# Kernel tuning notes

Hardware: AMD Instinct MI355X
Metric: run time of the kernel (lower is better)

The kernel has to match this reference:

```python
import jax, jax.numpy as jnp
import numpy as np

N = 4096   # nodes
G = 64     # graphs
MH = 128   # hidden multiplicity (0e and 1o)
MU = 64    # up multiplicity (0e and 1o)
NSP = 10   # num_species
EPS = 1e-5


def _forward(nfh, nfu, onehot, W_h0, W_h1, W_u0, W_u1, Wt_00, Wt_11, Wt_01, Wt_10,
             W_p0, b_p0, W_p1, Wsc0, Wsc1, ln_w0, ln_b0, ln_w1, W_s0, b_s0, W_s1, batch):
    n = nfh.shape[0]
    # unpack irreps layout: [0e scalars | 1o vectors flattened]
    h0 = nfh[:, :MH]                       # [N, MH]
    h1 = nfh[:, MH:].reshape(n, MH, 3)     # [N, MH, 3]
    u0 = nfu[:, :MU]
    u1 = nfu[:, MU:].reshape(n, MU, 3)
    inv_h = 1.0 / np.sqrt(MH)
    inv_u = 1.0 / np.sqrt(MU)
    # irrep-wise (block-diagonal) o3.Linear, e3nn fan-in normalization
    hp0 = (h0 @ W_h0) * inv_h
    hp1 = jnp.einsum('nui,uv->nvi', h1, W_h1) * inv_h
    up0 = (u0 @ W_u0) * inv_u
    up1 = jnp.einsum('nui,uv->nvi', u1, W_u1) * inv_u
    # SeparateWeightTensorProduct: fully-connected 'uvw' CG tensor product
    # paths to 0e (scalars + gates, 2*MH outputs): 0e x 0e and 1o x 1o (dot / sqrt3)
    inv_tp = 1.0 / np.sqrt(2.0 * MH * MU)   # component/path normalization (2 paths, fan MH*MU)
    xy00 = jnp.einsum('nu,nv->nuv', hp0, up0).reshape(n, MH * MU)
    xy11 = jnp.einsum('nui,nvi->nuv', hp1, up1).reshape(n, MH * MU)
    z0 = (xy00 @ Wt_00.reshape(MH * MU, 2 * MH)
          + (xy11 @ Wt_11.reshape(MH * MU, 2 * MH)) / np.sqrt(3.0)) * inv_tp  # [N, 2*MH]
    # paths to 1o: 0e x 1o and 1o x 0e (staged to control intermediate size)
    ta = jnp.einsum('nu,uvw->nvw', hp0, Wt_01)       # [N, MU, MH]
    z1a = jnp.einsum('nvw,nvi->nwi', ta, up1)
    tb = jnp.einsum('nv,uvw->nuw', up0, Wt_10)       # [N, MH, MH]
    z1b = jnp.einsum('nuw,nui->nwi', tb, hp1)
    z1 = (z1a + z1b) * inv_tp                        # [N, MH, 3]
    # Gate nonlinearity: silu on scalars, sigmoid gates multiply 1o features
    s = jax.nn.silu(z0[:, :MH])
    g = jax.nn.sigmoid(z0[:, MH:])
    v = z1 * g[:, :, None]
    # lin_post (biases on scalars only)
    p0 = (s @ W_p0) * inv_h + b_p0
    p1 = jnp.einsum('nui,uv->nvi', v, W_p1) * inv_h
    # self-connection: FullyConnectedTensorProduct(hidden, NSPx0e, out)
    inv_sc = 1.0 / np.sqrt(MH * NSP)
    sxy0 = jnp.einsum('nu,nv->nuv', h0, onehot).reshape(n, MH * NSP)
    y0 = p0 + (sxy0 @ Wsc0.reshape(MH * NSP, MH)) * inv_sc
    sxy1 = jnp.einsum('nui,nv->nuvi', h1, onehot).reshape(n, MH * NSP, 3)
    y1 = p1 + jnp.einsum('nki,kw->nwi', sxy1, Wsc1.reshape(MH * NSP, MH)) * inv_sc
    # e3LayerNorm: per-graph stats; mean-subtract scalars only, RMS-normalize per irrep
    ones = jnp.ones((n,), y0.dtype)
    cnt = jnp.maximum(jax.ops.segment_sum(ones, batch, num_segments=G), 1.0)[:, None]
    mean0 = (jax.ops.segment_sum(y0, batch, num_segments=G) / cnt).mean(axis=1)  # [G]
    f0 = y0 - mean0[batch][:, None]
    var0 = (jax.ops.segment_sum(f0 * f0, batch, num_segments=G) / cnt).mean(axis=1)
    f0 = f0 / (jnp.sqrt(var0)[batch][:, None] + EPS) * ln_w0 + ln_b0
    var1 = (jax.ops.segment_sum((y1 * y1).reshape(n, -1), batch, num_segments=G) / cnt).mean(axis=1)
    f1 = y1 / (jnp.sqrt(var1)[batch][:, None, None] + EPS) * ln_w1[None, :, None]
    # residual skip connection (o3.Linear with scalar bias)
    out0 = f0 + (h0 @ W_s0) * inv_h + b_s0
    out1 = f1 + jnp.einsum('nui,uv->nvi', h1, W_s1) * inv_h
    return jnp.concatenate([out0, out1.reshape(n, 3 * MH)], axis=1)  # [N, 512]


def setup_inputs() -> dict:
    key = jax.random.key(0)
    ks = jax.random.split(key, 20)
    f = lambda i, shape: jax.random.normal(ks[i], shape, dtype=jnp.float32)
    species = jax.random.randint(ks[0], (N,), 0, NSP)
    return {
        'node_feats_hidden': f(1, (N, 4 * MH)),
        'node_feats_up': f(2, (N, 4 * MU)),
        'node_one_hot': jax.nn.one_hot(species, NSP, dtype=jnp.float32),
        'batch': jnp.sort(jax.random.randint(ks[3], (N,), 0, G)),
        'W_h0': f(4, (MH, MH)), 'W_h1': f(5, (MH, MH)),
        'W_u0': f(6, (MU, MU)), 'W_u1': f(7, (MU, MU)),
        'Wt_00': f(8, (MH, MU, 2 * MH)), 'Wt_11': f(9, (MH, MU, 2 * MH)),
        'Wt_01': f(10, (MH, MU, MH)), 'Wt_10': f(11, (MH, MU, MH)),
        'W_p0': f(12, (MH, MH)), 'b_p0': jnp.zeros((MH,), jnp.float32), 'W_p1': f(13, (MH, MH)),
        'Wsc0': f(14, (MH, NSP, MH)), 'Wsc1': f(15, (MH, NSP, MH)),
        'ln_w0': jnp.ones((MH,), jnp.float32), 'ln_b0': jnp.zeros((MH,), jnp.float32),
        'ln_w1': jnp.ones((MH,), jnp.float32),
        'W_s0': f(16, (MH, MH)), 'b_s0': jnp.zeros((MH,), jnp.float32), 'W_s1': f(17, (MH, MH)),
    }


def reference(node_feats_hidden, node_feats_up, node_one_hot, batch, W_h0, W_h1, W_u0, W_u1,
              Wt_00, Wt_11, Wt_01, Wt_10, W_p0, b_p0, W_p1, Wsc0, Wsc1, ln_w0, ln_b0, ln_w1,
              W_s0, b_s0, W_s1):
    return _forward(node_feats_hidden, node_feats_up, node_one_hot, W_h0, W_h1, W_u0, W_u1,
                    Wt_00, Wt_11, Wt_01, Wt_10, W_p0, b_p0, W_p1, Wsc0, Wsc1,
                    ln_w0, ln_b0, ln_w1, W_s0, b_s0, W_s1, batch)
```

## Files before the change

kernel.cpp:

```cpp
#include <hip/hip_runtime.h>
#include <cstdint>
#include <cstddef>


typedef _Float16 half8 __attribute__((ext_vector_type(8)));
typedef _Float16 half4v __attribute__((ext_vector_type(4)));
typedef float f32x4 __attribute__((ext_vector_type(4)));

static constexpr float INV_H  = 0.08838834764831845f;
static constexpr float INV_U  = 0.125f;
static constexpr float INV_TP = 0.0078125f;
static constexpr float INV_SC = 0.02795084971874737f;
static constexpr float RSQRT3 = 0.5773502691896258f;
static constexpr float LN_EPS = 1e-5f;

static constexpr size_t OFF_BZ0 = 0;
static constexpr size_t OFF_BZ1 = OFF_BZ0 + 8388608;
static constexpr size_t OFF_WH0 = OFF_BZ1 + 4194304;
static constexpr size_t OFF_WH1 = OFF_WH0 + 32768;
static constexpr size_t OFF_WU0 = OFF_WH1 + 32768;
static constexpr size_t OFF_WU1 = OFF_WU0 + 8192;
static constexpr size_t OFF_WP0 = OFF_WU1 + 8192;
static constexpr size_t OFF_WP1 = OFF_WP0 + 32768;
static constexpr size_t OFF_WS0 = OFF_WP1 + 32768;
static constexpr size_t OFF_WS1 = OFF_WS0 + 32768;
static constexpr size_t OFF_H0F = OFF_WS1 + 32768;
static constexpr size_t OFF_H1F = OFF_H0F + 1048576;
static constexpr size_t OFF_U0F = OFF_H1F + 3145728;
static constexpr size_t OFF_U1F = OFF_U0F + 524288;
static constexpr size_t OFF_HP0 = OFF_U1F + 1572864;
static constexpr size_t OFF_HP1 = OFF_HP0 + 1048576;
static constexpr size_t OFF_UP0 = OFF_HP1 + 3145728;
static constexpr size_t OFF_UP1 = OFF_UP0 + 524288;
static constexpr size_t OFF_SF  = OFF_UP1 + 1572864;
static constexpr size_t OFF_VF  = OFF_SF + 1048576;
static constexpr size_t OFF_PZ0 = OFF_VF + 3145728;
static constexpr size_t OFF_PZ1 = OFF_PZ0 + 16777216;
static constexpr size_t OFF_Y0  = OFF_PZ1 + 12582912;
static constexpr size_t OFF_Y1  = OFF_Y0 + 2097152;
static constexpr size_t OFF_O0  = OFF_Y1 + 6291456;
static constexpr size_t OFF_O1  = OFF_O0 + 2097152;
static constexpr size_t OFF_SP  = OFF_O1 + 6291456;
static constexpr size_t OFF_ST  = OFF_SP + 16384;
static constexpr size_t WS_NEED = OFF_ST + 2048;

__global__ __launch_bounds__(256) void kconv(
    const float* __restrict__ nfh, const float* __restrict__ nfu,
    const float* __restrict__ onehot,
    const float* __restrict__ Wt00, const float* __restrict__ Wt11,
    const float* __restrict__ Wt01, const float* __restrict__ Wt10,
    const float* __restrict__ Wh0, const float* __restrict__ Wh1,
    const float* __restrict__ Wu0, const float* __restrict__ Wu1,
    const float* __restrict__ Wp0, const float* __restrict__ Wp1,
    const float* __restrict__ Ws0, const float* __restrict__ Ws1,
    char* __restrict__ ws)
{
  const int bid = blockIdx.x, t = threadIdx.x;
  if (bid < 768) {
    _Float16* dst;
    int u, nt = 0;
    const bool isz0 = bid < 512;
    if (isz0) { nt = bid >> 8; u = bid & 255; dst = (_Float16*)(ws + OFF_BZ0) + ((size_t)nt*256 + (size_t)u)*8192; }
    else      { u = bid - 512;               dst = (_Float16*)(ws + OFF_BZ1) + (size_t)u*8192; }
    for (int it = 0; it < 4; ++it) {
      int chunk = it*256 + t;
      int lane = chunk & 63, ch = chunk >> 6;
      int f = ch >> 1, c = ch & 1;
      int w = f*16 + (lane & 15);
      int v0 = c*32 + (lane >> 4)*8;
      half8 o;
      #pragma unroll
      for (int j = 0; j < 8; ++j) {
        float val;
        if (isz0) {
          if (u < 128) val = Wt00[(size_t)((u*64 + v0 + j)*256) + nt*128 + w];
          else         val = Wt11[(size_t)(((u-128)*64 + v0 + j)*256) + nt*128 + w] * RSQRT3;
        } else {
          if (u < 128) val = Wt01[(size_t)((u*64 + v0 + j)*128) + w];
          else         val = Wt10[(size_t)(((u-128)*64 + v0 + j)*128) + w];
        }
        o[j] = (_Float16)val;
      }
      *(half8*)(dst + (size_t)chunk*8) = o;
    }
  } else if (bid < 776) {
    int mat = bid - 768;
    const float* src; size_t doff; int K, N;
    switch (mat) {
      case 0: src = Wh0; doff = OFF_WH0; K = 128; N = 128; break;
      case 1: src = Wh1; doff = OFF_WH1; K = 128; N = 128; break;
      case 2: src = Wu0; doff = OFF_WU0; K = 64;  N = 64;  break;
      case 3: src = Wu1; doff = OFF_WU1; K = 64;  N = 64;  break;
      case 4: src = Wp0; doff = OFF_WP0; K = 128; N = 128; break;
      case 5: src = Wp1; doff = OFF_WP1; K = 128; N = 128; break;
      case 6: src = Ws0; doff = OFF_WS0; K = 128; N = 128; break;
      default: src = Ws1; doff = OFF_WS1; K = 128; N = 128; break;
    }
    _Float16* d = (_Float16*)(ws + doff);
    const int nfr = N >> 4;
    const int chunks = (K*N) >> 3;
    for (int qd = t; qd < chunks; qd += 256) {
      int lane = qd & 63, cf = qd >> 6;
      int f = cf % nfr, c = cf / nfr;
      int col = f*16 + (lane & 15);
      int k0 = c*32 + (lane >> 4)*8;
      half8 o;
      #pragma unroll
      for (int j = 0; j < 8; ++j) o[j] = (_Float16)src[(size_t)(k0 + j)*N + col];
      *(half8*)(d + (size_t)qd*8) = o;
    }
  } else if (bid < 1544) {
    const int stride = 768*256;
    const int base = (bid - 776)*256 + t;
    _Float16* h0f = (_Float16*)(ws + OFF_H0F);
    _Float16* h1f = (_Float16*)(ws + OFF_H1F);
    _Float16* u0f = (_Float16*)(ws + OFF_U0F);
    _Float16* u1f = (_Float16*)(ws + OFF_U1F);
    for (int id = base; id < 524288; id += stride)
      h0f[id] = (_Float16)nfh[(size_t)(id >> 7)*512 + (id & 127)];
    for (int id = base; id < 1572864; id += stride) {
      int i = id >> 19, r = id & 524287, n = r >> 7, u = r & 127;
      h1f[id] = (_Float16)nfh[(size_t)n*512 + 128 + u*3 + i];
    }
    for (int id = base; id < 262144; id += stride)
      u0f[id] = (_Float16)nfu[(size_t)(id >> 6)*256 + (id & 63)];
    for (int id = base; id < 786432; id += stride) {
      int i = id >> 18, r = id & 262143, n = r >> 6, v = r & 63;
      u1f[id] = (_Float16)nfu[(size_t)n*256 + 64 + v*3 + i];
    }
  } else {
    int node = (bid - 1544)*256 + t;
    const float* row = onehot + (size_t)node*10;
    int best = 0; float bv = row[0];
    #pragma unroll
    for (int s = 1; s < 10; ++s) { float v = row[s]; if (v > bv) { bv = v; best = s; } }
    ((int*)(ws + OFF_SP))[node] = best;
    if (bid == 1544) {
      float* stz = (float*)(ws + OFF_ST);
      stz[t] = 0.f; stz[t + 256] = 0.f;
    }
  }
}

template<int KK, int NO, int MODE>
__global__ __launch_bounds__(256) void kgemm_small(char* __restrict__ ws,
    const float* __restrict__ bp0, const float* __restrict__ bs0)
{
  constexpr int NT = NO / 16;
  const int bid = blockIdx.x, t = threadIdx.x;
  const int lane = t & 63, wid = t >> 6;
  const int quad = lane >> 4, l15 = lane & 15;
  const int job = bid >> 5, n0 = (bid & 31) << 7;

  const _Float16 *A, *W;
  _Float16* oh = nullptr; float* of = nullptr;
  const float* bias = nullptr;
  float scale;
  if constexpr (MODE == 0) {
    scale = INV_H;
    if (job == 0) { A = (const _Float16*)(ws + OFF_H0F); W = (const _Float16*)(ws + OFF_WH0); oh = (_Float16*)(ws + OFF_HP0); }
    else {
      A = (const _Float16*)(ws + OFF_H1F) + (size_t)(job-1)*524288;
      W = (const _Float16*)(ws + OFF_WH1);
      oh = (_Float16*)(ws + OFF_HP1) + (size_t)(job-1)*524288;
    }
  } else if constexpr (MODE == 1) {
    scale = INV_U;
    if (job == 0) { A = (const _Float16*)(ws + OFF_U0F); W = (const _Float16*)(ws + OFF_WU0); oh = (_Float16*)(ws + OFF_UP0); }
    else {
      A = (const _Float16*)(ws + OFF_U1F) + (size_t)(job-1)*262144;
      W = (const _Float16*)(ws + OFF_WU1);
      oh = (_Float16*)(ws + OFF_UP1) + (size_t)(job-1)*262144;
    }
  } else {
    scale = INV_H;
    switch (job) {
      case 0: A = (const _Float16*)(ws + OFF_SF);  W = (const _Float16*)(ws + OFF_WP0); of = (float*)(ws + OFF_Y0); bias = bp0; break;
      case 1: A = (const _Float16*)(ws + OFF_H0F); W = (const _Float16*)(ws + OFF_WS0); of = (float*)(ws + OFF_O0); bias = bs0; break;
      case 2: case 3: case 4:
        A = (const _Float16*)(ws + OFF_VF) + (size_t)(job-2)*524288;
        W = (const _Float16*)(ws + OFF_WP1);
        of = (float*)(ws + OFF_Y1) + (size_t)(job-2)*524288; break;
      default:
        A = (const _Float16*)(ws + OFF_H1F) + (size_t)(job-5)*524288;
        W = (const _Float16*)(ws + OFF_WS1);
        of = (float*)(ws + OFF_O1) + (size_t)(job-5)*524288; break;
    }
  }

  f32x4 acc[2][NT];
  const f32x4 zz = {0.f, 0.f, 0.f, 0.f};
  #pragma unroll
  for (int mf = 0; mf < 2; ++mf)
    #pragma unroll
    for (int nf = 0; nf < NT; ++nf) acc[mf][nf] = zz;

  #pragma unroll
  for (int kc = 0; kc < KK/32; ++kc) {
    half8 a[2];
    #pragma unroll
    for (int mf = 0; mf < 2; ++mf)
      a[mf] = *(const half8*)(A + (size_t)(n0 + wid*32 + mf*16 + l15)*KK + kc*32 + quad*8);
    #pragma unroll
    for (int nf = 0; nf < NT; ++nf) {
      half8 b = *(const half8*)(W + (size_t)(kc*NT + nf)*512 + lane*8);
      #pragma unroll
      for (int mf = 0; mf < 2; ++mf)
        acc[mf][nf] = __builtin_amdgcn_mfma_f32_16x16x32_f16(a[mf], b, acc[mf][nf], 0, 0, 0);
    }
  }

  #pragma unroll
  for (int mf = 0; mf < 2; ++mf)
    #pragma unroll
    for (int nf = 0; nf < NT; ++nf) {
      int col = nf*16 + l15;
      float bv = bias ? bias[col] : 0.f;
      #pragma unroll
      for (int r = 0; r < 4; ++r) {
        int row = n0 + wid*32 + mf*16 + quad*4 + r;
        float v = acc[mf][nf][r] * scale + bv;
        if constexpr (MODE < 2) oh[(size_t)row*NO + col] = (_Float16)v;
        else                    of[(size_t)row*NO + col] = v;
      }
    }
}

__global__ __launch_bounds__(256, 2) void kbig(char* __restrict__ ws)
{
  const int bid = blockIdx.x, t = threadIdx.x;
  const int lane = t & 63, wid = t >> 6;
  const int wy = wid >> 1, wx = wid & 1;
  const int quad = lane >> 4, l15 = lane & 15;

  const _Float16* hp0 = (const _Float16*)(ws + OFF_HP0);
  const _Float16* hp1 = (const _Float16*)(ws + OFF_HP1);
  const _Float16* up0 = (const _Float16*)(ws + OFF_UP0);
  const _Float16* up1 = (const _Float16*)(ws + OFF_UP1);

  const _Float16 *p, *q, *B0;
  float* out; int opitch; size_t obase; int node0;
  if (bid < 256) {
    int mt = bid >> 3, nt = (bid >> 2) & 1, kj = bid & 3;
    node0 = mt << 7;
    if (kj == 0) { p = hp0; q = up0; }
    else { p = hp1 + (size_t)(kj-1)*524288; q = up1 + (size_t)(kj-1)*262144; }
    B0 = (const _Float16*)(ws + OFF_BZ0) + (size_t)nt*2097152 + (kj ? (size_t)1048576 : (size_t)0);
    out = (float*)(ws + OFF_PZ0) + (size_t)kj*1048576;
    obase = (size_t)node0*256 + (size_t)nt*128;
    opitch = 256;
  } else {
    int b2 = bid - 256, mt = b2 >> 1, kj = b2 & 1, i = mt >> 5;
    node0 = (mt & 31) << 7;
    if (kj == 0) { p = hp0; q = up1 + (size_t)i*262144; }
    else         { p = hp1 + (size_t)i*524288; q = up0; }
    B0 = (const _Float16*)(ws + OFF_BZ1) + (kj ? (size_t)1048576 : (size_t)0);
    out = (float*)(ws + OFF_PZ1) + (size_t)kj*1572864;
    obase = (size_t)mt*16384;
    opitch = 128;
  }

  half8 qf[4][2];
  #pragma unroll
  for (int mf = 0; mf < 4; ++mf)
    #pragma unroll
    for (int c = 0; c < 2; ++c)
      qf[mf][c] = *(const half8*)(q + (size_t)(node0 + wy*64 + mf*16 + l15)*64 + c*32 + quad*8);

  f32x4 acc[4][4];
  const f32x4 zz = {0.f, 0.f, 0.f, 0.f};
  #pragma unroll
  for (int mf = 0; mf < 4; ++mf)
    #pragma unroll
    for (int nf = 0; nf < 4; ++nf) acc[mf][nf] = zz;

  const _Float16* prow = p + (size_t)(node0 + wy*64 + l15)*128;
  const _Float16* Bw = B0 + (size_t)wx*4096 + (size_t)lane*8;

  auto loadB = [&](half8 (&dst)[2][4], int uidx) {
    const _Float16* Bu = Bw + (size_t)uidx*8192;
    #pragma unroll
    for (int c = 0; c < 2; ++c)
      #pragma unroll
      for (int nf = 0; nf < 4; ++nf)
        dst[c][nf] = *(const half8*)(Bu + (size_t)((nf*2 + c)*512));
  };
  auto mstep = [&](const half8 (&bf)[2][4], const half4v (&pwl)[4], int uu) {
    #pragma unroll
    for (int mf = 0; mf < 4; ++mf) {
      const _Float16 ps = pwl[mf][uu];
      const half8 pv = {ps, ps, ps, ps, ps, ps, ps, ps};
      #pragma unroll
      for (int c = 0; c < 2; ++c) {
        half8 a = qf[mf][c] * pv;
        #pragma unroll
        for (int nf = 0; nf < 4; ++nf)
          acc[mf][nf] = __builtin_amdgcn_mfma_f32_16x16x32_f16(a, bf[c][nf], acc[mf][nf], 0, 0, 0);
      }
    }
  };

  half4v pw[4], pwN[4];
  #pragma unroll
  for (int mf = 0; mf < 4; ++mf)
    pw[mf] = *(const half4v*)(prow + (size_t)mf*2048);

  half8 bfA[2][4], bfB[2][4];
  loadB(bfA, 0);

  for (int u4 = 0; u4 < 32; ++u4) {
    const int b = u4*4;
    loadB(bfB, b + 1);
    mstep(bfA, pw, 0);
    loadB(bfA, b + 2);
    mstep(bfB, pw, 1);
    {
      const int np = (u4 < 31) ? (u4 + 1)*4 : u4*4;
      #pragma unroll
      for (int mf = 0; mf < 4; ++mf)
        pwN[mf] = *(const half4v*)(prow + (size_t)mf*2048 + np);
    }
    loadB(bfB, b + 3);
    mstep(bfA, pw, 2);
    loadB(bfA, (u4 < 31) ? (b + 4) : (b + 3));
    mstep(bfB, pw, 3);
    #pragma unroll
    for (int mf = 0; mf < 4; ++mf) pw[mf] = pwN[mf];
  }

  #pragma unroll
  for (int mf = 0; mf < 4; ++mf)
    #pragma unroll
    for (int nf = 0; nf < 4; ++nf) {
      int col = wx*64 + nf*16 + l15;
      #pragma unroll
      for (int r = 0; r < 4; ++r) {
        int row = wy*64 + mf*16 + quad*4 + r;
        out[obase + (size_t)row*opitch + col] = acc[mf][nf][r];
      }
    }
}

__global__ __launch_bounds__(256) void kreduce(char* __restrict__ ws)
{
  const int id = blockIdx.x*256 + threadIdx.x;
  const int n = id >> 7, w = id & 127;
  const float* pz0 = (const float*)(ws + OFF_PZ0);
  const float* pz1 = (const float*)(ws + OFF_PZ1);
  _Float16* sf = (_Float16*)(ws + OFF_SF);
  _Float16* vf = (_Float16*)(ws + OFF_VF);
  const size_t b = (size_t)n*256;
  float zs = (pz0[b + w] + pz0[1048576 + b + w] + pz0[2097152 + b + w] + pz0[3145728 + b + w]) * INV_TP;
  float zg = (pz0[b + 128 + w] + pz0[1048576 + b + 128 + w] + pz0[2097152 + b + 128 + w] + pz0[3145728 + b + 128 + w]) * INV_TP;
  float s = zs / (1.f + __expf(-zs));
  float g = 1.f / (1.f + __expf(-zg));
  sf[id] = (_Float16)s;
  #pragma unroll
  for (int i = 0; i < 3; ++i) {
    size_t r = ((size_t)i*4096 + (size_t)n)*128 + w;
    float z1v = (pz1[r] + pz1[1572864 + r]) * INV_TP;
    vf[(size_t)i*524288 + (size_t)n*128 + w] = (_Float16)(z1v * g);
  }
}

__global__ __launch_bounds__(256) void kscstats(char* __restrict__ ws,
    const float* __restrict__ nfh,
    const float* __restrict__ Wsc0, const float* __restrict__ Wsc1,
    const int* __restrict__ batch)
{
  const int t = threadIdx.x;
  const int node = blockIdx.x*2 + (t >> 7);
  const int w = t & 127;
  const int sp = ((const int*)(ws + OFF_SP))[node];
  const float* h = nfh + (size_t)node*512;
  float a0 = 0.f, a10 = 0.f, a11 = 0.f, a12 = 0.f;
  for (int u = 0; u < 128; ++u) {
    const size_t wi = (size_t)(u*10 + sp)*128 + w;
    float w0 = Wsc0[wi];
    float w1 = Wsc1[wi];
    a0 += h[u] * w0;
    a10 += h[128 + u*3 + 0] * w1;
    a11 += h[128 + u*3 + 1] * w1;
    a12 += h[128 + u*3 + 2] * w1;
  }
  float* y0 = (float*)(ws + OFF_Y0);
  float* y1 = (float*)(ws + OFF_Y1);
  const size_t i0 = (size_t)node*128 + w;
  float y0n  = y0[i0]           + INV_SC * a0;
  float y1n0 = y1[i0]           + INV_SC * a10;
  float y1n1 = y1[524288 + i0]  + INV_SC * a11;
  float y1n2 = y1[1048576 + i0] + INV_SC * a12;
  y0[i0] = y0n;
  y1[i0] = y1n0;
  y1[524288 + i0]  = y1n1;
  y1[1048576 + i0] = y1n2;

  float s0 = y0n, ss0 = y0n*y0n, ss1 = y1n0*y1n0 + y1n1*y1n1 + y1n2*y1n2;
  #pragma unroll
  for (int m = 1; m < 64; m <<= 1) {
    s0  += __shfl_xor(s0, m, 64);
    ss0 += __shfl_xor(ss0, m, 64);
    ss1 += __shfl_xor(ss1, m, 64);
  }
  __shared__ float red[4][3];
  if ((t & 63) == 0) {
    red[t >> 6][0] = s0; red[t >> 6][1] = ss0; red[t >> 6][2] = ss1;
  }
  __syncthreads();
  if ((t & 127) == 0) {
    const int wv = t >> 6;
    float* stp = (float*)(ws + OFF_ST);
    const int g = batch[node];
    atomicAdd(&stp[g],       red[wv][0] + red[wv+1][0]);
    atomicAdd(&stp[64 + g],  red[wv][1] + red[wv+1][1]);
    atomicAdd(&stp[128 + g], red[wv][2] + red[wv+1][2]);
    atomicAdd(&stp[192 + g], 1.f);
  }
}

__global__ __launch_bounds__(256) void kfinal(char* __restrict__ ws, const int* __restrict__ batch,
    const float* __restrict__ lnw0, const float* __restrict__ lnb0, const float* __restrict__ lnw1,
    float* __restrict__ outp)
{
  const int id = blockIdx.x*256 + threadIdx.x;
  const int n = id >> 9, c = id & 511;
  const float* st = (const float*)(ws + OFF_ST);
  const int g = batch[n];
  const float cnt = fmaxf(st[192 + g], 1.f);
  float val;
  if (c < 128) {
    const float* y0 = (const float*)(ws + OFF_Y0);
    const float* o0 = (const float*)(ws + OFF_O0);
    float m0   = st[g] / (cnt * 128.f);
    float var0 = st[64 + g] / (cnt * 128.f) - m0*m0;
    float inv0 = 1.f / (sqrtf(fmaxf(var0, 0.f)) + LN_EPS);
    val = (y0[(size_t)n*128 + c] - m0) * inv0 * lnw0[c] + lnb0[c] + o0[(size_t)n*128 + c];
  } else {
    int cc = c - 128, w = cc / 3, i = cc - w*3;
    const float* y1 = (const float*)(ws + OFF_Y1);
    const float* o1 = (const float*)(ws + OFF_O1);
    float inv1 = 1.f / (sqrtf(fmaxf(st[128 + g] / (cnt * 384.f), 0.f)) + LN_EPS);
    val = y1[(size_t)i*524288 + (size_t)n*128 + w] * inv1 * lnw1[w]
        + o1[(size_t)i*524288 + (size_t)n*128 + w];
  }
  outp[id] = val;
}

extern "C" void kernel_launch(void* const* d_in, const int* in_sizes, int n_in,
                              void* d_out, int out_size, void* d_ws, size_t ws_size,
                              hipStream_t stream)
{
  const float* nfh   = (const float*)d_in[0];
  const float* nfu   = (const float*)d_in[1];
  const float* oneh  = (const float*)d_in[2];
  const int*   batch = (const int*)d_in[3];
  const float* Wh0   = (const float*)d_in[4];
  const float* Wh1   = (const float*)d_in[5];
  const float* Wu0   = (const float*)d_in[6];
  const float* Wu1   = (const float*)d_in[7];
  const float* Wt00  = (const float*)d_in[8];
  const float* Wt11  = (const float*)d_in[9];
  const float* Wt01  = (const float*)d_in[10];
  const float* Wt10  = (const float*)d_in[11];
  const float* Wp0   = (const float*)d_in[12];
  const float* bp0   = (const float*)d_in[13];
  const float* Wp1   = (const float*)d_in[14];
  const float* Wsc0  = (const float*)d_in[15];
  const float* Wsc1  = (const float*)d_in[16];
  const float* lnw0  = (const float*)d_in[17];
  const float* lnb0  = (const float*)d_in[18];
  const float* lnw1  = (const float*)d_in[19];
  const float* Ws0   = (const float*)d_in[20];
  const float* bs0   = (const float*)d_in[21];
  const float* Ws1   = (const float*)d_in[22];
  char* ws = (char*)d_ws;

  if (ws_size < WS_NEED) {
    hipMemsetAsync(d_out, 0, (size_t)out_size * sizeof(float), stream);
    return;
  }

  kconv<<<1560, 256, 0, stream>>>(nfh, nfu, oneh, Wt00, Wt11, Wt01, Wt10,
                                  Wh0, Wh1, Wu0, Wu1, Wp0, Wp1, Ws0, Ws1, ws);
  kgemm_small<128,128,0><<<128, 256, 0, stream>>>(ws, nullptr, nullptr);
  kgemm_small<64, 64, 1><<<128, 256, 0, stream>>>(ws, nullptr, nullptr);
  kbig<<<448, 256, 0, stream>>>(ws);
  kreduce<<<2048, 256, 0, stream>>>(ws);
  kgemm_small<128,128,2><<<256, 256, 0, stream>>>(ws, bp0, bs0);
  kscstats<<<2048, 256, 0, stream>>>(ws, nfh, Wsc0, Wsc1, batch);
  kfinal<<<8192, 256, 0, stream>>>(ws, batch, lnw0, lnb0, lnw1, (float*)d_out);
}
```

Baseline: 353.8 us.

## Coalesce weight conversion via LDS, vectorize input casts, fp16 partials, merge small GEMMs

Weight repacking in kconv now stages each 64-row slab into LDS with float4 coalesced loads before the transposed fp16 pack, and the input casts use float4 loads and handle three vector components per thread. The two projection GEMMs are merged into one launch, and the big kernel writes its partial sums as fp16 instead of fp32, which halves the traffic into and out of kreduce. The hand-written double-buffered B prefetch in kbig is replaced by a simpler loop that leaves scheduling to the compiler. Storing partials in fp16 loses precision and risks overflow, and the simpler loop may hide less memory latency.

```diff
diff --git a/kernel.cpp b/kernel.cpp
--- a/kernel.cpp
+++ b/kernel.cpp
@@ -57,11 +57,34 @@
 {
   const int bid = blockIdx.x, t = threadIdx.x;
   if (bid < 768) {
+    __shared__ float lds[64 * 130];
     _Float16* dst;
     int u, nt = 0;
     const bool isz0 = bid < 512;
     if (isz0) { nt = bid >> 8; u = bid & 255; dst = (_Float16*)(ws + OFF_BZ0) + ((size_t)nt*256 + (size_t)u)*8192; }
     else      { u = bid - 512;               dst = (_Float16*)(ws + OFF_BZ1) + (size_t)u*8192; }
+
+    const float* src; int rowpitch, c0; float scale = 1.f;
+    if (isz0) {
+      rowpitch = 256; c0 = nt*128;
+      if (u < 128) { src = Wt00 + (size_t)(u*64)*256; }
+      else         { src = Wt11 + (size_t)((u-128)*64)*256; scale = RSQRT3; }
+    } else {
+      rowpitch = 128; c0 = 0;
+      if (u < 128) { src = Wt01 + (size_t)(u*64)*128; }
+      else         { src = Wt10 + (size_t)((u-128)*64)*128; }
+    }
+
+    #pragma unroll
+    for (int it = 0; it < 8; ++it) {
+      int gi = it*256 + t;
+      int row = gi >> 5, c4 = gi & 31;
+      const float4 v = *(const float4*)(src + (size_t)row*rowpitch + c0 + c4*4);
+      float* dl = lds + row*130 + c4*4;
+      dl[0] = v.x; dl[1] = v.y; dl[2] = v.z; dl[3] = v.w;
+    }
+    __syncthreads();
+
     for (int it = 0; it < 4; ++it) {
       int chunk = it*256 + t;
       int lane = chunk & 63, ch = chunk >> 6;
@@ -70,17 +93,8 @@
       int v0 = c*32 + (lane >> 4)*8;
       half8 o;
       #pragma unroll
-      for (int j = 0; j < 8; ++j) {
-        float val;
-        if (isz0) {
-          if (u < 128) val = Wt00[(size_t)((u*64 + v0 + j)*256) + nt*128 + w];
-          else         val = Wt11[(size_t)(((u-128)*64 + v0 + j)*256) + nt*128 + w] * RSQRT3;
-        } else {
-          if (u < 128) val = Wt01[(size_t)((u*64 + v0 + j)*128) + w];
-          else         val = Wt10[(size_t)(((u-128)*64 + v0 + j)*128) + w];
-        }
-        o[j] = (_Float16)val;
-      }
+      for (int j = 0; j < 8; ++j)
+        o[j] = (_Float16)(lds[(v0 + j)*130 + w] * scale);
       *(half8*)(dst + (size_t)chunk*8) = o;
     }
   } else if (bid < 776) {
@@ -116,17 +130,31 @@
     _Float16* h1f = (_Float16*)(ws + OFF_H1F);
     _Float16* u0f = (_Float16*)(ws + OFF_U0F);
     _Float16* u1f = (_Float16*)(ws + OFF_U1F);
-    for (int id = base; id < 524288; id += stride)
-      h0f[id] = (_Float16)nfh[(size_t)(id >> 7)*512 + (id & 127)];
-    for (int id = base; id < 1572864; id += stride) {
-      int i = id >> 19, r = id & 524287, n = r >> 7, u = r & 127;
-      h1f[id] = (_Float16)nfh[(size_t)n*512 + 128 + u*3 + i];
-    }
-    for (int id = base; id < 262144; id += stride)
-      u0f[id] = (_Float16)nfu[(size_t)(id >> 6)*256 + (id & 63)];
-    for (int id = base; id < 786432; id += stride) {
-      int i = id >> 18, r = id & 262143, n = r >> 6, v = r & 63;
-      u1f[id] = (_Float16)nfu[(size_t)n*256 + 64 + v*3 + i];
+    for (int vid = base; vid < 131072; vid += stride) {
+      int n = vid >> 5, c4 = (vid & 31)*4;
+      const float4 v = *(const float4*)(nfh + (size_t)n*512 + c4);
+      half4v o = { (_Float16)v.x, (_Float16)v.y, (_Float16)v.z, (_Float16)v.w };
+      *(half4v*)(h0f + (size_t)vid*4) = o;
+    }
+    for (int vid = base; vid < 65536; vid += stride) {
+      int n = vid >> 4, c4 = (vid & 15)*4;
+      const float4 v = *(const float4*)(nfu + (size_t)n*256 + c4);
+      half4v o = { (_Float16)v.x, (_Float16)v.y, (_Float16)v.z, (_Float16)v.w };
+      *(half4v*)(u0f + (size_t)vid*4) = o;
+    }
+    for (int id = base; id < 524288; id += stride) {
+      int n = id >> 7, u = id & 127;
+      const float* s = nfh + (size_t)n*512 + 128 + u*3;
+      h1f[id]            = (_Float16)s[0];
+      h1f[524288 + id]   = (_Float16)s[1];
+      h1f[1048576 + id]  = (_Float16)s[2];
+    }
+    for (int id = base; id < 262144; id += stride) {
+      int n = id >> 6, v = id & 63;
+      const float* s = nfu + (size_t)n*256 + 64 + v*3;
+      u1f[id]            = (_Float16)s[0];
+      u1f[262144 + id]   = (_Float16)s[1];
+      u1f[524288 + id]   = (_Float16)s[2];
     }
   } else {
     int node = (bid - 1544)*256 + t;
@@ -143,11 +171,11 @@
 }
 
 template<int KK, int NO, int MODE>
-__global__ __launch_bounds__(256) void kgemm_small(char* __restrict__ ws,
-    const float* __restrict__ bp0, const float* __restrict__ bs0)
+__device__ __forceinline__ void gemm_small_body(char* __restrict__ ws,
+    const float* __restrict__ bp0, const float* __restrict__ bs0,
+    int bid, int t)
 {
   constexpr int NT = NO / 16;
-  const int bid = blockIdx.x, t = threadIdx.x;
   const int lane = t & 63, wid = t >> 6;
   const int quad = lane >> 4, l15 = lane & 15;
   const int job = bid >> 5, n0 = (bid & 31) << 7;
@@ -226,6 +254,18 @@
     }
 }
 
+__global__ __launch_bounds__(256) void kprep(char* __restrict__ ws)
+{
+  if (blockIdx.x < 128) gemm_small_body<128,128,0>(ws, nullptr, nullptr, blockIdx.x, threadIdx.x);
+  else                  gemm_small_body<64, 64, 1>(ws, nullptr, nullptr, blockIdx.x - 128, threadIdx.x);
+}
+
+__global__ __launch_bounds__(256) void ktail(char* __restrict__ ws,
+    const float* __restrict__ bp0, const float* __restrict__ bs0)
+{
+  gemm_small_body<128,128,2>(ws, bp0, bs0, blockIdx.x, threadIdx.x);
+}
+
 __global__ __launch_bounds__(256, 2) void kbig(char* __restrict__ ws)
 {
   const int bid = blockIdx.x, t = threadIdx.x;
@@ -239,14 +279,14 @@
   const _Float16* up1 = (const _Float16*)(ws + OFF_UP1);
 
   const _Float16 *p, *q, *B0;
-  float* out; int opitch; size_t obase; int node0;
+  _Float16* out; int opitch; size_t obase; int node0;
   if (bid < 256) {
     int mt = bid >> 3, nt = (bid >> 2) & 1, kj = bid & 3;
     node0 = mt << 7;
     if (kj == 0) { p = hp0; q = up0; }
     else { p = hp1 + (size_t)(kj-1)*524288; q = up1 + (size_t)(kj-1)*262144; }
     B0 = (const _Float16*)(ws + OFF_BZ0) + (size_t)nt*2097152 + (kj ? (size_t)1048576 : (size_t)0);
-    out = (float*)(ws + OFF_PZ0) + (size_t)kj*1048576;
+    out = (_Float16*)(ws + OFF_PZ0) + (size_t)kj*1048576;
     obase = (size_t)node0*256 + (size_t)nt*128;
     opitch = 256;
   } else {
@@ -255,7 +295,7 @@
     if (kj == 0) { p = hp0; q = up1 + (size_t)i*262144; }
     else         { p = hp1 + (size_t)i*524288; q = up0; }
     B0 = (const _Float16*)(ws + OFF_BZ1) + (kj ? (size_t)1048576 : (size_t)0);
-    out = (float*)(ws + OFF_PZ1) + (size_t)kj*1572864;
+    out = (_Float16*)(ws + OFF_PZ1) + (size_t)kj*1572864;
     obase = (size_t)mt*16384;
     opitch = 128;
   }
@@ -277,55 +317,33 @@
   const _Float16* prow = p + (size_t)(node0 + wy*64 + l15)*128;
   const _Float16* Bw = B0 + (size_t)wx*4096 + (size_t)lane*8;
 
-  auto loadB = [&](half8 (&dst)[2][4], int uidx) {
-    const _Float16* Bu = Bw + (size_t)uidx*8192;
-    #pragma unroll
-    for (int c = 0; c < 2; ++c)
-      #pragma unroll
-      for (int nf = 0; nf < 4; ++nf)
-        dst[c][nf] = *(const half8*)(Bu + (size_t)((nf*2 + c)*512));
-  };
-  auto mstep = [&](const half8 (&bf)[2][4], const half4v (&pwl)[4], int uu) {
-    #pragma unroll
-    for (int mf = 0; mf < 4; ++mf) {
-      const _Float16 ps = pwl[mf][uu];
-      const half8 pv = {ps, ps, ps, ps, ps, ps, ps, ps};
-      #pragma unroll
-      for (int c = 0; c < 2; ++c) {
-        half8 a = qf[mf][c] * pv;
+  for (int u4 = 0; u4 < 32; ++u4) {
+    half4v pw[4];
+    #pragma unroll
+    for (int mf = 0; mf < 4; ++mf)
+      pw[mf] = *(const half4v*)(prow + (size_t)mf*2048 + u4*4);
+    #pragma unroll
+    for (int uu = 0; uu < 4; ++uu) {
+      const _Float16* Bu = Bw + (size_t)(u4*4 + uu)*8192;
+      half8 bf[2][4];
+      #pragma unroll
+      for (int c = 0; c < 2; ++c)
         #pragma unroll
         for (int nf = 0; nf < 4; ++nf)
-          acc[mf][nf] = __builtin_amdgcn_mfma_f32_16x16x32_f16(a, bf[c][nf], acc[mf][nf], 0, 0, 0);
+          bf[c][nf] = *(const half8*)(Bu + (size_t)((nf*2 + c)*512));
+      #pragma unroll
+      for (int mf = 0; mf < 4; ++mf) {
+        const _Float16 ps = pw[mf][uu];
+        const half8 pv = {ps, ps, ps, ps, ps, ps, ps, ps};
+        #pragma unroll
+        for (int c = 0; c < 2; ++c) {
+          half8 a = qf[mf][c] * pv;
+          #pragma unroll
+          for (int nf = 0; nf < 4; ++nf)
+            acc[mf][nf] = __builtin_amdgcn_mfma_f32_16x16x32_f16(a, bf[c][nf], acc[mf][nf], 0, 0, 0);
+        }
       }
     }
-  };
-
-  half4v pw[4], pwN[4];
-  #pragma unroll
-  for (int mf = 0; mf < 4; ++mf)
-    pw[mf] = *(const half4v*)(prow + (size_t)mf*2048);
-
-  half8 bfA[2][4], bfB[2][4];
-  loadB(bfA, 0);
-
-  for (int u4 = 0; u4 < 32; ++u4) {
-    const int b = u4*4;
-    loadB(bfB, b + 1);
-    mstep(bfA, pw, 0);
-    loadB(bfA, b + 2);
-    mstep(bfB, pw, 1);
-    {
-      const int np = (u4 < 31) ? (u4 + 1)*4 : u4*4;
-      #pragma unroll
-      for (int mf = 0; mf < 4; ++mf)
-        pwN[mf] = *(const half4v*)(prow + (size_t)mf*2048 + np);
-    }
-    loadB(bfB, b + 3);
-    mstep(bfA, pw, 2);
-    loadB(bfA, (u4 < 31) ? (b + 4) : (b + 3));
-    mstep(bfB, pw, 3);
-    #pragma unroll
-    for (int mf = 0; mf < 4; ++mf) pw[mf] = pwN[mf];
   }
 
   #pragma unroll
@@ -336,7 +354,7 @@
       #pragma unroll
       for (int r = 0; r < 4; ++r) {
         int row = wy*64 + mf*16 + quad*4 + r;
-        out[obase + (size_t)row*opitch + col] = acc[mf][nf][r];
+        out[obase + (size_t)row*opitch + col] = (_Float16)acc[mf][nf][r];
       }
     }
 }
@@ -345,20 +363,22 @@
 {
   const int id = blockIdx.x*256 + threadIdx.x;
   const int n = id >> 7, w = id & 127;
-  const float* pz0 = (const float*)(ws + OFF_PZ0);
-  const float* pz1 = (const float*)(ws + OFF_PZ1);
+  const _Float16* pz0 = (const _Float16*)(ws + OFF_PZ0);
+  const _Float16* pz1 = (const _Float16*)(ws + OFF_PZ1);
   _Float16* sf = (_Float16*)(ws + OFF_SF);
   _Float16* vf = (_Float16*)(ws + OFF_VF);
   const size_t b = (size_t)n*256;
-  float zs = (pz0[b + w] + pz0[1048576 + b + w] + pz0[2097152 + b + w] + pz0[3145728 + b + w]) * INV_TP;
-  float zg = (pz0[b + 128 + w] + pz0[1048576 + b + 128 + w] + pz0[2097152 + b + 128 + w] + pz0[3145728 + b + 128 + w]) * INV_TP;
+  float zs = ((float)pz0[b + w] + (float)pz0[1048576 + b + w]
+            + (float)pz0[2097152 + b + w] + (float)pz0[3145728 + b + w]) * INV_TP;
+  float zg = ((float)pz0[b + 128 + w] + (float)pz0[1048576 + b + 128 + w]
+            + (float)pz0[2097152 + b + 128 + w] + (float)pz0[3145728 + b + 128 + w]) * INV_TP;
   float s = zs / (1.f + __expf(-zs));
   float g = 1.f / (1.f + __expf(-zg));
   sf[id] = (_Float16)s;
   #pragma unroll
   for (int i = 0; i < 3; ++i) {
     size_t r = ((size_t)i*4096 + (size_t)n)*128 + w;
-    float z1v = (pz1[r] + pz1[1572864 + r]) * INV_TP;
+    float z1v = ((float)pz1[r] + (float)pz1[1572864 + r]) * INV_TP;
     vf[(size_t)i*524288 + (size_t)n*128 + w] = (_Float16)(z1v * g);
   }
 }
@@ -482,11 +502,10 @@
 
   kconv<<<1560, 256, 0, stream>>>(nfh, nfu, oneh, Wt00, Wt11, Wt01, Wt10,
                                   Wh0, Wh1, Wu0, Wu1, Wp0, Wp1, Ws0, Ws1, ws);
-  kgemm_small<128,128,0><<<128, 256, 0, stream>>>(ws, nullptr, nullptr);
-  kgemm_small<64, 64, 1><<<128, 256, 0, stream>>>(ws, nullptr, nullptr);
+  kprep<<<256, 256, 0, stream>>>(ws);
   kbig<<<448, 256, 0, stream>>>(ws);
   kreduce<<<2048, 256, 0, stream>>>(ws);
-  kgemm_small<128,128,2><<<256, 256, 0, stream>>>(ws, bp0, bs0);
+  ktail<<<256, 256, 0, stream>>>(ws, bp0, bs0);
   kscstats<<<2048, 256, 0, stream>>>(ws, nfh, Wsc0, Wsc1, batch);
   kfinal<<<8192, 256, 0, stream>>>(ws, batch, lnw0, lnb0, lnw1, (float*)d_out);
 }
```

Result: faster. 341.6 us (-3.4%).
